# Kernel tuning notes

Hardware: AMD Instinct MI355X
Metric: run time of the kernel (lower is better)

## Reference

```python
import jax, jax.numpy as jnp
import numpy as np

B, T, M, C, H = 2, 2048, 512, 512, 8
D = C // H
SCALE = 1.0 / np.sqrt(D).astype(np.float32)


def _linear_params(key, din, dout):
    kw, kb = jax.random.split(key)
    W = jax.random.normal(kw, (din, dout), jnp.float32) * 0.02
    b = jax.random.normal(kb, (dout,), jnp.float32) * 0.02
    return W, b


def setup_inputs() -> dict:
    key = jax.random.key(0)
    ks = jax.random.split(key, 8)
    x = jax.random.normal(ks[0], (B, T, C), jnp.float32)
    y = jax.random.normal(ks[1], (B, M, C), jnp.float32)
    # causal mask over the x (self / product-attn) axis, broadcasts to [B,H,T,T]
    attn_x_mask = jnp.tril(jnp.ones((T, T), jnp.int32))[None, None]
    Wqkv_x, bqkv_x = _linear_params(ks[2], C, 3 * C)
    Wqkv_y, bqkv_y = _linear_params(ks[3], C, 3 * C)
    Wgs, bgs = _linear_params(ks[4], C, C)
    Wgc, bgc = _linear_params(ks[5], C, C)
    Wp, bp = _linear_params(ks[6], C, C)
    return dict(x=x, y=y, attn_x_mask=attn_x_mask,
                Wqkv_x=Wqkv_x, bqkv_x=bqkv_x, Wqkv_y=Wqkv_y, bqkv_y=bqkv_y,
                Wgs=Wgs, bgs=bgs, Wgc=Wgc, bgc=bgc, Wp=Wp, bp=bp)


def _heads(t, L):
    # [B,L,C] -> [B,H,L,D]
    return t.reshape(B, L, H, D).transpose(0, 2, 1, 3)


def reference(x, y, attn_x_mask, Wqkv_x, bqkv_x, Wqkv_y, bqkv_y,
              Wgs, bgs, Wgc, bgc, Wp, bp):
    neg_inf = jnp.float32(-jnp.inf)
    qx, kx, vx = jnp.split(x @ Wqkv_x + bqkv_x, 3, axis=-1)
    qy, ky, vy = jnp.split(y @ Wqkv_y + bqkv_y, 3, axis=-1)
    q_x, k_x, v_x = _heads(qx, T), _heads(kx, T), _heads(vx, T)
    q_y, k_y, v_y = _heads(qy, M), _heads(ky, M), _heads(vy, M)

    # cross attention x -> y : [B,H,T,M]
    catt_x2y = jnp.einsum('bhtd,bhmd->bhtm', q_x, k_y) * SCALE
    cval_x2y = jnp.einsum('bhtm,bhmd->bhtd', jax.nn.softmax(catt_x2y, axis=-1), v_y)
    cval_x2y = cval_x2y.transpose(0, 2, 1, 3).reshape(B, T, C)

    # product attention: (x->y scores) @ (y->x scores) : [B,H,T,T]
    catt_y2x = jnp.einsum('bhmd,bhtd->bhmt', q_y, k_x) * SCALE
    prod = jnp.einsum('bhtm,bhms->bhts', catt_x2y, catt_y2x) * SCALE
    prod = jnp.where(attn_x_mask == 0, neg_inf, prod)
    cval_y2x = jnp.einsum('bhts,bhsd->bhtd', jax.nn.softmax(prod, axis=-1), v_x)
    cval_y2x = cval_y2x.transpose(0, 2, 1, 3).reshape(B, T, C)

    cval = cval_x2y + cval_y2x

    # self attention on x : [B,H,T,T]
    satt = jnp.einsum('bhtd,bhsd->bhts', q_x, k_x) * SCALE
    satt = jnp.where(attn_x_mask == 0, neg_inf, satt)
    sval = jnp.einsum('bhts,bhsd->bhtd', jax.nn.softmax(satt, axis=-1), v_x)
    sval = sval.transpose(0, 2, 1, 3).reshape(B, T, C)

    sgate = jax.nn.sigmoid(sval @ Wgs + bgs)
    cgate = jax.nn.sigmoid(cval @ Wgc + bgc)
    out = (sgate * cval + cgate * sval) @ Wp + bp
    return out
```

## Files before the change

### kernel.cpp

```cpp
#include <hip/hip_runtime.h>
#include <hip/hip_bf16.h>

typedef unsigned short ushort_t;
typedef __attribute__((ext_vector_type(8))) short s8v;
typedef __attribute__((ext_vector_type(4))) float f4;
typedef __attribute__((ext_vector_type(4))) unsigned short u16x4;

#define BB 2
#define TT 2048
#define MMM 512
#define CC 512
#define HH 8
#define DD 64
#define SCALE 0.125f
#define SCALE_L2E 0.18033688011112042f

__device__ __forceinline__ ushort_t f2bf(float v) {
    __hip_bfloat16 h = __float2bfloat16(v);
    return *reinterpret_cast<ushort_t*>(&h);
}
__device__ __forceinline__ float bf2f(ushort_t u) {
    __hip_bfloat16 h;
    *reinterpret_cast<ushort_t*>(&h) = u;
    return __bfloat162float(h);
}
__device__ __forceinline__ float exp2_raw(float v) {
    float p;
    asm("v_exp_f32 %0, %1" : "=v"(p) : "v"(v));
    return p;
}

__device__ __forceinline__ void gload16(const void* g, void* l) {
    __builtin_amdgcn_global_load_lds((const __attribute__((address_space(1))) void*)g,
                                     (__attribute__((address_space(3))) void*)l, 16, 0, 0);
}

__device__ __forceinline__ void transp32(const float* W, ushort_t* WT, int K, int N,
                                         int bx, int by, int tid) {
    const int k0 = by * 32, n0 = bx * 32;
    __shared__ float t[32][33];
    for (int i = tid; i < 1024; i += 256) {
        int r = i >> 5, c = i & 31;
        t[r][c] = W[(long)(k0 + r) * N + n0 + c];
    }
    __syncthreads();
    for (int i = tid; i < 1024; i += 256) {
        int r = i >> 5, c = i & 31;
        WT[(long)(n0 + r) * K + k0 + c] = f2bf(t[c][r]);
    }
}
__device__ __forceinline__ void cvt4(const float* s, ushort_t* d, long blk, int tid) {
    long i = (blk * 256 + tid) * 4;
    float4 v = *(const float4*)(s + i);
    u16x4 o;
    o[0] = f2bf(v.x); o[1] = f2bf(v.y); o[2] = f2bf(v.z); o[3] = f2bf(v.w);
    *(u16x4*)(d + i) = o;
}

__global__ __launch_bounds__(256) void prep_k(
    const float* __restrict__ x, const float* __restrict__ y,
    const float* __restrict__ Wqx, const float* __restrict__ Wqy,
    const float* __restrict__ Wgs, const float* __restrict__ Wgc,
    const float* __restrict__ Wp,
    ushort_t* __restrict__ xb, ushort_t* __restrict__ yb,
    ushort_t* __restrict__ WqxT, ushort_t* __restrict__ WqyT,
    ushort_t* __restrict__ WgsT, ushort_t* __restrict__ WgcT,
    ushort_t* __restrict__ WpT)
{
    const int bid = blockIdx.x, tid = threadIdx.x;
    if (bid < 2048)      cvt4(x, xb, bid, tid);
    else if (bid < 2560) cvt4(y, yb, bid - 2048, tid);
    else if (bid < 3328) { int l = bid - 2560; transp32(Wqx, WqxT, 512, 1536, l % 48, l / 48, tid); }
    else if (bid < 4096) { int l = bid - 3328; transp32(Wqy, WqyT, 512, 1536, l % 48, l / 48, tid); }
    else if (bid < 4352) { int l = bid - 4096; transp32(Wgs, WgsT, 512, 512, l % 16, l / 16, tid); }
    else if (bid < 4608) { int l = bid - 4352; transp32(Wgc, WgcT, 512, 512, l % 16, l / 16, tid); }
    else                 { int l = bid - 4608; transp32(Wp, WpT, 512, 512, l % 16, l / 16, tid); }
}

__global__ __launch_bounds__(256) void vT_fused(
    const ushort_t* __restrict__ qkvx, const ushort_t* __restrict__ qkvy,
    ushort_t* __restrict__ vxT, ushort_t* __restrict__ vyT,
    ushort_t* __restrict__ kyT, ushort_t* __restrict__ qyT)
{
    const int bx = blockIdx.x, z = blockIdx.y, b = z >> 3, h = z & 7;
    const ushort_t* src; ushort_t* dst; int S, s0; long sB, dZ;
    if (bx < 32)      { src = qkvx + 1024; dst = vxT; S = TT;  sB = (long)TT * 1536;  dZ = (long)64 * TT;  s0 = bx * 64; }
    else if (bx < 40) { src = qkvy + 1024; dst = vyT; S = MMM; sB = (long)MMM * 1536; dZ = (long)64 * MMM; s0 = (bx - 32) * 64; }
    else if (bx < 48) { src = qkvy + 512;  dst = kyT; S = MMM; sB = (long)MMM * 1536; dZ = (long)64 * MMM; s0 = (bx - 40) * 64; }
    else              { src = qkvy;        dst = qyT; S = MMM; sB = (long)MMM * 1536; dZ = (long)64 * MMM; s0 = (bx - 48) * 64; }
    const ushort_t* sp = src + (long)b * sB + (long)h * 64;
    ushort_t* dp = dst + (long)z * dZ;
    __shared__ ushort_t t[64][65];
    for (int i = threadIdx.x; i < 4096; i += 256) {
        int r = i >> 6, c = i & 63;
        t[r][c] = sp[(long)(s0 + r) * 1536 + c];
    }
    __syncthreads();
    for (int i = threadIdx.x; i < 4096; i += 256) {
        int d = i >> 6, c = i & 63;
        dp[(long)d * S + s0 + c] = t[c][d];
    }
}

__global__ __launch_bounds__(256) void qkv_k(
    const ushort_t* __restrict__ xb, const ushort_t* __restrict__ yb,
    const ushort_t* __restrict__ WqxT, const ushort_t* __restrict__ WqyT,
    const float* __restrict__ bqx, const float* __restrict__ bqy,
    ushort_t* __restrict__ qkvx, ushort_t* __restrict__ qkvy)
{
    const int by = blockIdx.y;
    const ushort_t* A; const ushort_t* Bm; const float* bias; ushort_t* O;
    int r0, qcols;
    if (by < 32) { A = xb; Bm = WqxT; bias = bqx; O = qkvx; r0 = by * 128; qcols = 512; }
    else         { A = yb; Bm = WqyT; bias = bqy; O = qkvy; r0 = (by - 32) * 128; qcols = 0; }
    const int c0 = blockIdx.x * 128;
    const int tid = threadIdx.x, w = tid >> 6, lane = tid & 63;
    const int quad = lane >> 4, l15 = lane & 15;
    const int rowBase = (w >> 1) * 64, colBase = (w & 1) * 64;

    __shared__ __align__(16) ushort_t Al[128 * 64];
    __shared__ __align__(16) ushort_t Bl[128 * 64];

    f4 acc[4][4] = {};

    for (int k0 = 0; k0 < 512; k0 += 64) {
        __syncthreads();
        for (int n = 0; n < 4; ++n) {
            int f = w * 4096 + n * 1024 + lane * 16;
            int row = f >> 7;
            int blk_g = ((f & 127) >> 4) ^ (row & 7);
            gload16(A + (long)(r0 + row) * 512 + k0 + blk_g * 8,
                    &Al[(w * 4096 + n * 1024) >> 1]);
            gload16(Bm + (long)(c0 + row) * 512 + k0 + blk_g * 8,
                    &Bl[(w * 4096 + n * 1024) >> 1]);
        }
        __syncthreads();
#pragma unroll
        for (int ks = 0; ks < 2; ++ks) {
            s8v af[4], bfr[4];
#pragma unroll
            for (int i = 0; i < 4; ++i) {
                int row = rowBase + 16 * i + l15;
                af[i] = *(const s8v*)&Al[row * 64 + (((ks * 4 + quad) ^ (row & 7)) * 8)];
                int col = colBase + 16 * i + l15;
                bfr[i] = *(const s8v*)&Bl[col * 64 + (((ks * 4 + quad) ^ (col & 7)) * 8)];
            }
#pragma unroll
            for (int i = 0; i < 4; ++i)
#pragma unroll
                for (int j = 0; j < 4; ++j)
                    acc[i][j] = __builtin_amdgcn_mfma_f32_16x16x32_bf16(af[i], bfr[j], acc[i][j], 0, 0, 0);
        }
    }

#pragma unroll
    for (int i = 0; i < 4; ++i)
#pragma unroll
        for (int j = 0; j < 4; ++j)
#pragma unroll
            for (int r = 0; r < 4; ++r) {
                int row = r0 + rowBase + 16 * i + quad * 4 + r;
                int col = c0 + colBase + 16 * j + l15;
                float v = acc[i][j][r] + bias[col];
                if (col < qcols) v *= SCALE_L2E;
                O[(long)row * 1536 + col] = f2bf(v);
            }
}

__global__ __launch_bounds__(256) void proj_k(
    const ushort_t* __restrict__ A, const ushort_t* __restrict__ Bm,
    float* __restrict__ O, const float* __restrict__ bias)
{
    const int r0 = blockIdx.y * 128, c0 = blockIdx.x * 64;
    const int tid = threadIdx.x, w = tid >> 6, lane = tid & 63;
    const int quad = lane >> 4, l15 = lane & 15;
    const int rowBase = (w >> 1) * 64, colBase = (w & 1) * 32;

    __shared__ __align__(16) ushort_t Al[128 * 64];
    __shared__ __align__(16) ushort_t Bl[64 * 64];

    f4 acc[4][2] = {};

    for (int k0 = 0; k0 < 512; k0 += 64) {
        __syncthreads();
#pragma unroll
        for (int n = 0; n < 4; ++n) {
            int f = w * 4096 + n * 1024 + lane * 16;
            int row = f >> 7;
            int blk_g = ((f & 127) >> 4) ^ (row & 7);
            gload16(A + (long)(r0 + row) * 512 + k0 + blk_g * 8,
                    &Al[(w * 4096 + n * 1024) >> 1]);
        }
#pragma unroll
        for (int n = 0; n < 2; ++n) {
            int f = w * 2048 + n * 1024 + lane * 16;
            int row = f >> 7;
            int blk_g = ((f & 127) >> 4) ^ (row & 7);
            gload16(Bm + (long)(c0 + row) * 512 + k0 + blk_g * 8,
                    &Bl[(w * 2048 + n * 1024) >> 1]);
        }
        __syncthreads();
#pragma unroll
        for (int ks = 0; ks < 2; ++ks) {
            s8v af[4], bfr[2];
#pragma unroll
            for (int i = 0; i < 4; ++i) {
                int row = rowBase + 16 * i + l15;
                af[i] = *(const s8v*)&Al[row * 64 + (((ks * 4 + quad) ^ (row & 7)) * 8)];
            }
#pragma unroll
            for (int j = 0; j < 2; ++j) {
                int col = colBase + 16 * j + l15;
                bfr[j] = *(const s8v*)&Bl[col * 64 + (((ks * 4 + quad) ^ (col & 7)) * 8)];
            }
#pragma unroll
            for (int i = 0; i < 4; ++i)
#pragma unroll
                for (int j = 0; j < 2; ++j)
                    acc[i][j] = __builtin_amdgcn_mfma_f32_16x16x32_bf16(af[i], bfr[j], acc[i][j], 0, 0, 0);
        }
    }

#pragma unroll
    for (int i = 0; i < 4; ++i)
#pragma unroll
        for (int j = 0; j < 2; ++j)
#pragma unroll
            for (int r = 0; r < 4; ++r) {
                int row = r0 + rowBase + 16 * i + quad * 4 + r;
                int col = c0 + colBase + 16 * j + l15;
                O[(long)row * 512 + col] = acc[i][j][r] + bias[col];
            }
}

__global__ __launch_bounds__(256) void gt_k(const ushort_t* __restrict__ qyT,
                                            const ushort_t* __restrict__ kyT,
                                            ushort_t* __restrict__ Gt)
{
    const int z = blockIdx.x;
    const int tid = threadIdx.x, w = tid >> 6, lane = tid & 63;
    const int quad = lane >> 4, l15 = lane & 15;
    const ushort_t* A  = qyT + (long)z * 64 * MMM;
    const ushort_t* Bm = kyT + (long)z * 64 * MMM;
    __shared__ float red[4][4096];
    f4 acc[4][4] = {};
    for (int kk = 0; kk < 4; ++kk) {
        const int ks = w * 4 + kk;
        s8v af[4], bfr[4];
#pragma unroll
        for (int i = 0; i < 4; ++i) {
            af[i]  = *(const s8v*)(A  + (long)(16 * i + l15) * MMM + ks * 32 + quad * 8);
            bfr[i] = *(const s8v*)(Bm + (long)(16 * i + l15) * MMM + ks * 32 + quad * 8);
        }
#pragma unroll
        for (int i = 0; i < 4; ++i)
#pragma unroll
            for (int j = 0; j < 4; ++j)
                acc[i][j] = __builtin_amdgcn_mfma_f32_16x16x32_bf16(af[i], bfr[j], acc[i][j], 0, 0, 0);
    }
#pragma unroll
    for (int i = 0; i < 4; ++i)
#pragma unroll
        for (int j = 0; j < 4; ++j)
            *(f4*)&red[w][(i * 4 + j) * 256 + lane * 4] = acc[i][j];
    __syncthreads();
    const float s2 = SCALE * SCALE;
#pragma unroll
    for (int j = 0; j < 4; ++j) {
        f4 s = *(const f4*)&red[0][(w * 4 + j) * 256 + lane * 4];
#pragma unroll
        for (int ww = 1; ww < 4; ++ww)
            s += *(const f4*)&red[ww][(w * 4 + j) * 256 + lane * 4];
#pragma unroll
        for (int r = 0; r < 4; ++r) {
            int d2 = 16 * w + quad * 4 + r, d1 = 16 * j + l15;
            Gt[(long)z * 4096 + d2 * 64 + d1] = f2bf(s2 * s[r]);
        }
    }
}

__device__ __forceinline__ void stage_k64(const ushort_t* src, long rstride, int s0,
                                          ushort_t* Kl, int w, int lane) {
#pragma unroll
    for (int n = 0; n < 2; ++n) {
        int f = w * 2048 + n * 1024 + lane * 16;
        int row = f >> 7;
        int krow = ((row & 15) << 2) | (row >> 4);
        int blk = ((f & 127) >> 4) ^ (row & 7);
        gload16(src + (long)(s0 + krow) * rstride + blk * 8, &Kl[(w * 2048 + n * 1024) >> 1]);
    }
}
__device__ __forceinline__ void stage_v64(const ushort_t* src, long rstride, int s0,
                                          ushort_t* Vl, int w, int lane) {
#pragma unroll
    for (int n = 0; n < 2; ++n) {
        int f = w * 2048 + n * 1024 + lane * 16;
        int row = f >> 7;
        int blk = ((f & 127) >> 4) ^ (row & 7);
        gload16(src + (long)row * rstride + s0 + blk * 8, &Vl[(w * 2048 + n * 1024) >> 1]);
    }
}
__device__ __forceinline__ void qk8(f4 Sc[4], const s8v qf[2], const ushort_t* Kl,
                                    int quad, int l15) {
    __builtin_amdgcn_s_setprio(1);
#pragma unroll
    for (int ks = 0; ks < 2; ++ks)
#pragma unroll
        for (int c = 0; c < 4; ++c) {
            int row = 16 * c + l15;
            s8v bb = *(const s8v*)&Kl[row * 64 + (((ks * 4 + quad) ^ (row & 7)) * 8)];
            Sc[c] = __builtin_amdgcn_mfma_f32_16x16x32_bf16(qf[ks], bb, Sc[c], 0, 0, 0);
        }
    __builtin_amdgcn_s_setprio(0);
}
__device__ __forceinline__ void qk8_dual(f4 Ss[4], f4 Sp[4], const s8v qa[2], const s8v qb[2],
                                         const ushort_t* Kl, int quad, int l15) {
    __builtin_amdgcn_s_setprio(1);
#pragma unroll
    for (int ks = 0; ks < 2; ++ks)
#pragma unroll
        for (int c = 0; c < 4; ++c) {
            int row = 16 * c + l15;
            s8v bb = *(const s8v*)&Kl[row * 64 + (((ks * 4 + quad) ^ (row & 7)) * 8)];
            Ss[c] = __builtin_amdgcn_mfma_f32_16x16x32_bf16(qa[ks], bb, Ss[c], 0, 0, 0);
            Sp[c] = __builtin_amdgcn_mfma_f32_16x16x32_bf16(qb[ks], bb, Sp[c], 0, 0, 0);
        }
    __builtin_amdgcn_s_setprio(0);
}
__device__ __forceinline__ void smax0(const f4 Sc[4], float l_i[4], ushort_t* PlW,
                                      int diag, int trow0, int s0, int quad, int l15) {
#pragma unroll
    for (int r = 0; r < 4; ++r) {
        const int trow = trow0 + quad * 4 + r;
        u16x4 o;
#pragma unroll
        for (int c = 0; c < 4; ++c) {
            float v = Sc[c][r];
            if (diag && (s0 + 4 * l15 + c) > trow) v = -3e38f;
            float p = exp2_raw(v);
            l_i[r] += p;
            o[c] = f2bf(p);
        }
        *(u16x4*)&PlW[(quad * 4 + r) * 72 + 4 * l15] = o;
    }
}
__device__ __forceinline__ void pv8(f4 Oc[4], const ushort_t* PlW, const ushort_t* Vl,
                                    int quad, int l15) {
    __builtin_amdgcn_s_setprio(1);
#pragma unroll
    for (int ks = 0; ks < 2; ++ks) {
        s8v a = *(const s8v*)&PlW[l15 * 72 + ks * 32 + quad * 8];
#pragma unroll
        for (int c = 0; c < 4; ++c) {
            int row = 16 * c + l15;
            s8v bb = *(const s8v*)&Vl[row * 64 + (((ks * 4 + quad) ^ (row & 7)) * 8)];
            Oc[c] = __builtin_amdgcn_mfma_f32_16x16x32_bf16(a, bb, Oc[c], 0, 0, 0);
        }
    }
    __builtin_amdgcn_s_setprio(0);
}
__device__ __forceinline__ void pv8_dual(f4 Os[4], f4 Op[4], const ushort_t* Ps,
                                         const ushort_t* Pp, const ushort_t* Vl,
                                         int quad, int l15) {
    __builtin_amdgcn_s_setprio(1);
#pragma unroll
    for (int ks = 0; ks < 2; ++ks) {
        s8v as = *(const s8v*)&Ps[l15 * 72 + ks * 32 + quad * 8];
        s8v ap = *(const s8v*)&Pp[l15 * 72 + ks * 32 + quad * 8];
#pragma unroll
        for (int c = 0; c < 4; ++c) {
            int row = 16 * c + l15;
            s8v bb = *(const s8v*)&Vl[row * 64 + (((ks * 4 + quad) ^ (row & 7)) * 8)];
            Os[c] = __builtin_amdgcn_mfma_f32_16x16x32_bf16(as, bb, Os[c], 0, 0, 0);
            Op[c] = __builtin_amdgcn_mfma_f32_16x16x32_bf16(ap, bb, Op[c], 0, 0, 0);
        }
    }
    __builtin_amdgcn_s_setprio(0);
}

__global__ __launch_bounds__(256, 2) void flash_fused(
    const ushort_t* __restrict__ qkvx, const ushort_t* __restrict__ qkvy,
    const ushort_t* __restrict__ Gt, const ushort_t* __restrict__ vxT,
    const ushort_t* __restrict__ vyT,
    ushort_t* __restrict__ cval, ushort_t* __restrict__ sval)
{
    const int z = blockIdx.y, b = z >> 3, h = z & 7;
    const ushort_t* qx = qkvx + (long)b * (TT * 1536) + h * 64;
    const ushort_t* kx = qx + 512;
    const ushort_t* ky = qkvy + (long)b * (MMM * 1536) + 512 + h * 64;
    const ushort_t* Gz = Gt + (long)z * 4096;
    const ushort_t* vx = vxT + (long)z * (64 * TT);
    const ushort_t* vy = vyT + (long)z * (64 * MMM);

    const int xw = (z & 8) ? (int)blockIdx.x : (int)(gridDim.x - 1 - blockIdx.x);
    const int t0 = xw * 64;
    const int tid = threadIdx.x, w = tid >> 6, lane = tid & 63;
    const int quad = lane >> 4, l15 = lane & 15;

    __shared__ __align__(16) ushort_t Kl[2][64 * 64];
    __shared__ __align__(16) ushort_t Vl[2][64 * 64];
    __shared__ __align__(16) ushort_t Pl[2][4 * 16 * 72];
    ushort_t* PlWs = &Pl[0][w * 1152];
    ushort_t* PlWp = &Pl[1][w * 1152];

    stage_k64(ky, 1536, 0, Kl[0], w, lane);
    stage_v64(vy, MMM, 0, Vl[0], w, lane);

    const int qrow = t0 + 16 * w + l15;
    s8v qfx[2], qft[2];
    qfx[0] = *(const s8v*)(qx + (long)qrow * 1536 + quad * 8);
    qfx[1] = *(const s8v*)(qx + (long)qrow * 1536 + 32 + quad * 8);
    {
        f4 qa[4] = {};
#pragma unroll
        for (int ks = 0; ks < 2; ++ks)
#pragma unroll
            for (int j = 0; j < 4; ++j) {
                s8v bb = *(const s8v*)(Gz + (4 * l15 + j) * 64 + ks * 32 + quad * 8);
                qa[j] = __builtin_amdgcn_mfma_f32_16x16x32_bf16(qfx[ks], bb, qa[j], 0, 0, 0);
            }
#pragma unroll
        for (int r = 0; r < 4; ++r) {
            u16x4 o;
#pragma unroll
            for (int j = 0; j < 4; ++j) o[j] = f2bf(qa[j][r]);
            *(u16x4*)&PlWs[(quad * 4 + r) * 72 + 4 * l15] = o;
        }
        qft[0] = *(const s8v*)&PlWs[l15 * 72 + quad * 8];
        qft[1] = *(const s8v*)&PlWs[l15 * 72 + 32 + quad * 8];
    }

    f4 Occ[4] = {}, Ocs[4] = {}, Ocp[4] = {};
    float lc[4] = {}, ls[4] = {}, lp[4] = {};

    const int nT1 = MMM / 64;
    const int nTiles = nT1 + t0 / 64 + 1;

    for (int ti = 0; ti < nTiles; ++ti) {
        const int bi = ti & 1;
        __syncthreads();
        if (ti + 1 < nTiles) {
            const int tn = ti + 1, bn = tn & 1;
            if (tn < nT1) {
                stage_k64(ky, 1536, tn * 64, Kl[bn], w, lane);
                stage_v64(vy, MMM, tn * 64, Vl[bn], w, lane);
            } else {
                const int s0n = (tn - nT1) * 64;
                stage_k64(kx, 1536, s0n, Kl[bn], w, lane);
                stage_v64(vx, TT, s0n, Vl[bn], w, lane);
            }
        }
        if (ti < nT1) {
            f4 Sc[4] = {};
            qk8(Sc, qfx, Kl[bi], quad, l15);
            smax0(Sc, lc, PlWs, 0, 0, 0, quad, l15);
            pv8(Occ, PlWs, Vl[bi], quad, l15);
        } else {
            const int s0 = (ti - nT1) * 64;
            const int diag = (s0 == t0);
            f4 Ss[4] = {}, Sp[4] = {};
            qk8_dual(Ss, Sp, qfx, qft, Kl[bi], quad, l15);
            smax0(Ss, ls, PlWs, diag, t0 + 16 * w, s0, quad, l15);
            smax0(Sp, lp, PlWp, diag, t0 + 16 * w, s0, quad, l15);
            pv8_dual(Ocs, Ocp, PlWs, PlWp, Vl[bi], quad, l15);
        }
    }

#pragma unroll
    for (int r = 0; r < 4; ++r)
#pragma unroll
        for (int mb = 1; mb < 16; mb <<= 1) {
            lc[r] += __shfl_xor(lc[r], mb, 64);
            ls[r] += __shfl_xor(ls[r], mb, 64);
            lp[r] += __shfl_xor(lp[r], mb, 64);
        }

    const long ob = (long)b * (TT * CC) + h * 64;
#pragma unroll
    for (int r = 0; r < 4; ++r) {
        int row = t0 + 16 * w + quad * 4 + r;
        float ic = 1.f / lc[r], ip = 1.f / lp[r], isv = 1.f / ls[r];
#pragma unroll
        for (int c = 0; c < 4; ++c) {
            long idx = ob + (long)row * CC + 16 * c + l15;
            cval[idx] = f2bf(Occ[c][r] * ic + Ocp[c][r] * ip);
            sval[idx] = f2bf(Ocs[c][r] * isv);
        }
    }
}

__global__ __launch_bounds__(256) void gate_gemm(
    const ushort_t* __restrict__ sval, const ushort_t* __restrict__ cvalb,
    const ushort_t* __restrict__ WgsT, const ushort_t* __restrict__ WgcT,
    const float* __restrict__ bgs, const float* __restrict__ bgc,
    ushort_t* __restrict__ tmpb)
{
    const int r0 = blockIdx.y * 128, c0 = blockIdx.x * 64;
    const int tid = threadIdx.x, w = tid >> 6, lane = tid & 63;
    const int quad = lane >> 4, l15 = lane & 15;
    const int rowBase = (w >> 1) * 64, colBase = (w & 1) * 32;

    __shared__ __align__(16) ushort_t Al[128 * 64];
    __shared__ __align__(16) ushort_t Bl[64 * 64];

    f4 acc1[4][2] = {}, acc2[4][2] = {};

    for (int pass = 0; pass < 2; ++pass) {
        const ushort_t* A = pass ? cvalb : sval;
        const ushort_t* Bm = pass ? WgcT : WgsT;
        for (int k0 = 0; k0 < 512; k0 += 64) {
            __syncthreads();
#pragma unroll
            for (int n = 0; n < 4; ++n) {
                int f = w * 4096 + n * 1024 + lane * 16;
                int row = f >> 7;
                int blk_g = ((f & 127) >> 4) ^ (row & 7);
                gload16(A + (long)(r0 + row) * 512 + k0 + blk_g * 8,
                        &Al[(w * 4096 + n * 1024) >> 1]);
            }
#pragma unroll
            for (int n = 0; n < 2; ++n) {
                int f = w * 2048 + n * 1024 + lane * 16;
                int row = f >> 7;
                int blk_g = ((f & 127) >> 4) ^ (row & 7);
                gload16(Bm + (long)(c0 + row) * 512 + k0 + blk_g * 8,
                        &Bl[(w * 2048 + n * 1024) >> 1]);
            }
            __syncthreads();
#pragma unroll
            for (int ks = 0; ks < 2; ++ks) {
                s8v af[4], bfr[2];
#pragma unroll
                for (int i = 0; i < 4; ++i) {
                    int row = rowBase + 16 * i + l15;
                    af[i] = *(const s8v*)&Al[row * 64 + (((ks * 4 + quad) ^ (row & 7)) * 8)];
                }
#pragma unroll
                for (int j = 0; j < 2; ++j) {
                    int col = colBase + 16 * j + l15;
                    bfr[j] = *(const s8v*)&Bl[col * 64 + (((ks * 4 + quad) ^ (col & 7)) * 8)];
                }
                if (pass == 0) {
#pragma unroll
                    for (int i = 0; i < 4; ++i)
#pragma unroll
                        for (int j = 0; j < 2; ++j)
                            acc1[i][j] = __builtin_amdgcn_mfma_f32_16x16x32_bf16(af[i], bfr[j], acc1[i][j], 0, 0, 0);
                } else {
#pragma unroll
                    for (int i = 0; i < 4; ++i)
#pragma unroll
                        for (int j = 0; j < 2; ++j)
                            acc2[i][j] = __builtin_amdgcn_mfma_f32_16x16x32_bf16(af[i], bfr[j], acc2[i][j], 0, 0, 0);
                }
            }
        }
    }

#pragma unroll
    for (int i = 0; i < 4; ++i)
#pragma unroll
        for (int j = 0; j < 2; ++j)
#pragma unroll
            for (int r = 0; r < 4; ++r) {
                int row = r0 + rowBase + 16 * i + quad * 4 + r;
                int col = c0 + colBase + 16 * j + l15;
                long idx = (long)row * 512 + col;
                float g1 = 1.f / (1.f + __expf(-(acc1[i][j][r] + bgs[col])));
                float g2 = 1.f / (1.f + __expf(-(acc2[i][j][r] + bgc[col])));
                tmpb[idx] = f2bf(g1 * bf2f(cvalb[idx]) + g2 * bf2f(sval[idx]));
            }
}

extern "C" void kernel_launch(void* const* d_in, const int* in_sizes, int n_in,
                              void* d_out, int out_size, void* d_ws, size_t ws_size,
                              hipStream_t stream) {
    const float* x      = (const float*)d_in[0];
    const float* y      = (const float*)d_in[1];
    const float* Wqkv_x = (const float*)d_in[3];
    const float* bqkv_x = (const float*)d_in[4];
    const float* Wqkv_y = (const float*)d_in[5];
    const float* bqkv_y = (const float*)d_in[6];
    const float* Wgs    = (const float*)d_in[7];
    const float* bgs    = (const float*)d_in[8];
    const float* Wgc    = (const float*)d_in[9];
    const float* bgc    = (const float*)d_in[10];
    const float* Wp     = (const float*)d_in[11];
    const float* bp     = (const float*)d_in[12];
    float* out = (float*)d_out;

    ushort_t* u = (ushort_t*)d_ws;
    long o = 0;
    ushort_t* xb    = u + o; o += (long)BB * TT * CC;
    ushort_t* yb    = u + o; o += (long)BB * MMM * CC;
    ushort_t* WqxT  = u + o; o += 1536L * 512;
    ushort_t* WqyT  = u + o; o += 1536L * 512;
    ushort_t* WgsT  = u + o; o += 512L * 512;
    ushort_t* WgcT  = u + o; o += 512L * 512;
    ushort_t* WpT   = u + o; o += 512L * 512;
    ushort_t* qkvx  = u + o; o += (long)BB * TT * 1536;
    ushort_t* qkvy  = u + o; o += (long)BB * MMM * 1536;
    ushort_t* vxT   = u + o; o += (long)BB * HH * DD * TT;
    ushort_t* vyT   = u + o; o += (long)BB * HH * DD * MMM;
    ushort_t* kyT   = u + o; o += (long)BB * HH * DD * MMM;
    ushort_t* qyT   = u + o; o += (long)BB * HH * DD * MMM;
    ushort_t* Gt    = u + o; o += 16L * 64 * 64;
    ushort_t* cvalb = u + o; o += (long)BB * TT * CC;
    ushort_t* sval  = u + o; o += (long)BB * TT * CC;
    ushort_t* tmpb  = u + o; o += (long)BB * TT * CC;

    dim3 blk(256);

    prep_k<<<dim3(4864), blk, 0, stream>>>(x, y, Wqkv_x, Wqkv_y, Wgs, Wgc, Wp,
                                           xb, yb, WqxT, WqyT, WgsT, WgcT, WpT);

    qkv_k<<<dim3(12, 40), blk, 0, stream>>>(xb, yb, WqxT, WqyT, bqkv_x, bqkv_y, qkvx, qkvy);

    vT_fused<<<dim3(56, 16), blk, 0, stream>>>(qkvx, qkvy, vxT, vyT, kyT, qyT);

    gt_k<<<dim3(16), blk, 0, stream>>>(qyT, kyT, Gt);

    flash_fused<<<dim3(32, 16), blk, 0, stream>>>(qkvx, qkvy, Gt, vxT, vyT, cvalb, sval);

    gate_gemm<<<dim3(8, 32), blk, 0, stream>>>(sval, cvalb, WgsT, WgcT, bgs, bgc, tmpb);

    proj_k<<<dim3(8, 32), blk, 0, stream>>>(tmpb, WpT, out, bp);
}
```

Measured before the change: 214.5 us.

## Pipeline GEMM and flash-attention staging with multi-buffered LDS and vectorized transposes

Adds double buffering to the QKV GEMM and triple-buffered LDS prefetch to the flash, gate and projection kernels. These use explicit vmcnt waits and raw barriers so global loads overlap MFMA work. The gate and projection GEMMs shrink to 64x64 tiles, doubling the grid to fill more CUs. The V/K/Q transpose kernel now uses 16-byte vector loads and stores with an XOR-swizzled LDS tile. More LDS per block may lower occupancy, and the hand-written vmcnt counts depend on the exact number of loads issued per stage.

```diff
diff --git a/kernel.cpp b/kernel.cpp
--- a/kernel.cpp
+++ b/kernel.cpp
@@ -90,15 +90,48 @@
     else              { src = qkvy;        dst = qyT; S = MMM; sB = (long)MMM * 1536; dZ = (long)64 * MMM; s0 = (bx - 48) * 64; }
     const ushort_t* sp = src + (long)b * sB + (long)h * 64;
     ushort_t* dp = dst + (long)z * dZ;
-    __shared__ ushort_t t[64][65];
-    for (int i = threadIdx.x; i < 4096; i += 256) {
-        int r = i >> 6, c = i & 63;
-        t[r][c] = sp[(long)(s0 + r) * 1536 + c];
+    __shared__ __align__(16) ushort_t t[64][80];
+    const int tid = threadIdx.x;
+#pragma unroll
+    for (int p = 0; p < 2; ++p) {
+        int id = tid + p * 256;
+        int r = id >> 3, cc = (id & 7) * 8;
+        int cs = cc ^ ((r >> 3) * 8);
+        *(s8v*)&t[r][cs] = *(const s8v*)&sp[(long)(s0 + r) * 1536 + cc];
     }
     __syncthreads();
-    for (int i = threadIdx.x; i < 4096; i += 256) {
-        int d = i >> 6, c = i & 63;
-        dp[(long)d * S + s0 + c] = t[c][d];
+#pragma unroll
+    for (int p = 0; p < 2; ++p) {
+        int id = tid + p * 256;
+        int d = id >> 3, cc = (id & 7) * 8;
+        s8v o;
+#pragma unroll
+        for (int k = 0; k < 8; ++k) {
+            int r = cc + k;
+            o[k] = (short)t[r][d ^ ((r >> 3) * 8)];
+        }
+        *(s8v*)&dp[(long)d * S + s0 + cc] = o;
+    }
+}
+
+__device__ __forceinline__ void stage_rows128(const ushort_t* src, long k0,
+                                              ushort_t* dstL, int w, int lane) {
+#pragma unroll
+    for (int n = 0; n < 4; ++n) {
+        int f = w * 4096 + n * 1024 + lane * 16;
+        int row = f >> 7;
+        int blk_g = ((f & 127) >> 4) ^ (row & 7);
+        gload16(src + (long)row * 512 + k0 + blk_g * 8, dstL + ((w * 4096 + n * 1024) >> 1));
+    }
+}
+__device__ __forceinline__ void stage_rows64(const ushort_t* src, long k0,
+                                             ushort_t* dstL, int w, int lane) {
+#pragma unroll
+    for (int n = 0; n < 2; ++n) {
+        int f = w * 2048 + n * 1024 + lane * 16;
+        int row = f >> 7;
+        int blk_g = ((f & 127) >> 4) ^ (row & 7);
+        gload16(src + (long)row * 512 + k0 + blk_g * 8, dstL + ((w * 2048 + n * 1024) >> 1));
     }
 }
 
@@ -118,32 +151,33 @@
     const int quad = lane >> 4, l15 = lane & 15;
     const int rowBase = (w >> 1) * 64, colBase = (w & 1) * 64;
 
-    __shared__ __align__(16) ushort_t Al[128 * 64];
-    __shared__ __align__(16) ushort_t Bl[128 * 64];
+    __shared__ __align__(16) ushort_t Al[2][128 * 64];
+    __shared__ __align__(16) ushort_t Bl[2][128 * 64];
+
+    const ushort_t* Ab = A + (long)r0 * 512;
+    const ushort_t* Bb = Bm + (long)c0 * 512;
 
     f4 acc[4][4] = {};
 
-    for (int k0 = 0; k0 < 512; k0 += 64) {
-        __syncthreads();
-        for (int n = 0; n < 4; ++n) {
-            int f = w * 4096 + n * 1024 + lane * 16;
-            int row = f >> 7;
-            int blk_g = ((f & 127) >> 4) ^ (row & 7);
-            gload16(A + (long)(r0 + row) * 512 + k0 + blk_g * 8,
-                    &Al[(w * 4096 + n * 1024) >> 1]);
-            gload16(Bm + (long)(c0 + row) * 512 + k0 + blk_g * 8,
-                    &Bl[(w * 4096 + n * 1024) >> 1]);
-        }
-        __syncthreads();
+    stage_rows128(Ab, 0, Al[0], w, lane);
+    stage_rows128(Bb, 0, Bl[0], w, lane);
+    __syncthreads();
+
+    for (int kk = 0; kk < 8; ++kk) {
+        const int cur = kk & 1;
+        if (kk < 7) {
+            stage_rows128(Ab, (kk + 1) * 64, Al[cur ^ 1], w, lane);
+            stage_rows128(Bb, (kk + 1) * 64, Bl[cur ^ 1], w, lane);
+        }
 #pragma unroll
         for (int ks = 0; ks < 2; ++ks) {
             s8v af[4], bfr[4];
 #pragma unroll
             for (int i = 0; i < 4; ++i) {
                 int row = rowBase + 16 * i + l15;
-                af[i] = *(const s8v*)&Al[row * 64 + (((ks * 4 + quad) ^ (row & 7)) * 8)];
+                af[i] = *(const s8v*)&Al[cur][row * 64 + (((ks * 4 + quad) ^ (row & 7)) * 8)];
                 int col = colBase + 16 * i + l15;
-                bfr[i] = *(const s8v*)&Bl[col * 64 + (((ks * 4 + quad) ^ (col & 7)) * 8)];
+                bfr[i] = *(const s8v*)&Bl[cur][col * 64 + (((ks * 4 + quad) ^ (col & 7)) * 8)];
             }
 #pragma unroll
             for (int i = 0; i < 4; ++i)
@@ -151,6 +185,7 @@
                 for (int j = 0; j < 4; ++j)
                     acc[i][j] = __builtin_amdgcn_mfma_f32_16x16x32_bf16(af[i], bfr[j], acc[i][j], 0, 0, 0);
         }
+        __syncthreads();
     }
 
 #pragma unroll
@@ -171,58 +206,55 @@
     const ushort_t* __restrict__ A, const ushort_t* __restrict__ Bm,
     float* __restrict__ O, const float* __restrict__ bias)
 {
-    const int r0 = blockIdx.y * 128, c0 = blockIdx.x * 64;
+    const int r0 = blockIdx.y * 64, c0 = blockIdx.x * 64;
     const int tid = threadIdx.x, w = tid >> 6, lane = tid & 63;
     const int quad = lane >> 4, l15 = lane & 15;
-    const int rowBase = (w >> 1) * 64, colBase = (w & 1) * 32;
-
-    __shared__ __align__(16) ushort_t Al[128 * 64];
-    __shared__ __align__(16) ushort_t Bl[64 * 64];
-
-    f4 acc[4][2] = {};
-
-    for (int k0 = 0; k0 < 512; k0 += 64) {
-        __syncthreads();
-#pragma unroll
-        for (int n = 0; n < 4; ++n) {
-            int f = w * 4096 + n * 1024 + lane * 16;
-            int row = f >> 7;
-            int blk_g = ((f & 127) >> 4) ^ (row & 7);
-            gload16(A + (long)(r0 + row) * 512 + k0 + blk_g * 8,
-                    &Al[(w * 4096 + n * 1024) >> 1]);
-        }
-#pragma unroll
-        for (int n = 0; n < 2; ++n) {
-            int f = w * 2048 + n * 1024 + lane * 16;
-            int row = f >> 7;
-            int blk_g = ((f & 127) >> 4) ^ (row & 7);
-            gload16(Bm + (long)(c0 + row) * 512 + k0 + blk_g * 8,
-                    &Bl[(w * 2048 + n * 1024) >> 1]);
-        }
-        __syncthreads();
+    const int rowBase = (w >> 1) * 32, colBase = (w & 1) * 32;
+
+    __shared__ __align__(16) ushort_t Al[3][64 * 64];
+    __shared__ __align__(16) ushort_t Bl[3][64 * 64];
+
+    const ushort_t* Ab = A + (long)r0 * 512;
+    const ushort_t* Bb = Bm + (long)c0 * 512;
+
+    f4 acc[2][2] = {};
+
+    stage_rows64(Ab, 0, Al[0], w, lane);
+    stage_rows64(Bb, 0, Bl[0], w, lane);
+    stage_rows64(Ab, 64, Al[1], w, lane);
+    stage_rows64(Bb, 64, Bl[1], w, lane);
+
+    int cur = 0;
+    for (int kk = 0; kk < 8; ++kk) {
+        if (kk + 1 < 8) asm volatile("s_waitcnt vmcnt(4)" ::: "memory");
+        else            asm volatile("s_waitcnt vmcnt(0)" ::: "memory");
+        asm volatile("s_barrier" ::: "memory");
+        if (kk + 2 < 8) {
+            int s = cur + 2; if (s >= 3) s -= 3;
+            stage_rows64(Ab, (kk + 2) * 64, Al[s], w, lane);
+            stage_rows64(Bb, (kk + 2) * 64, Bl[s], w, lane);
+        }
 #pragma unroll
         for (int ks = 0; ks < 2; ++ks) {
-            s8v af[4], bfr[2];
-#pragma unroll
-            for (int i = 0; i < 4; ++i) {
+            s8v af[2], bfr[2];
+#pragma unroll
+            for (int i = 0; i < 2; ++i) {
                 int row = rowBase + 16 * i + l15;
-                af[i] = *(const s8v*)&Al[row * 64 + (((ks * 4 + quad) ^ (row & 7)) * 8)];
-            }
-#pragma unroll
-            for (int j = 0; j < 2; ++j) {
-                int col = colBase + 16 * j + l15;
-                bfr[j] = *(const s8v*)&Bl[col * 64 + (((ks * 4 + quad) ^ (col & 7)) * 8)];
-            }
-#pragma unroll
-            for (int i = 0; i < 4; ++i)
+                af[i] = *(const s8v*)&Al[cur][row * 64 + (((ks * 4 + quad) ^ (row & 7)) * 8)];
+                int col = colBase + 16 * i + l15;
+                bfr[i] = *(const s8v*)&Bl[cur][col * 64 + (((ks * 4 + quad) ^ (col & 7)) * 8)];
+            }
+#pragma unroll
+            for (int i = 0; i < 2; ++i)
 #pragma unroll
                 for (int j = 0; j < 2; ++j)
                     acc[i][j] = __builtin_amdgcn_mfma_f32_16x16x32_bf16(af[i], bfr[j], acc[i][j], 0, 0, 0);
         }
-    }
-
-#pragma unroll
-    for (int i = 0; i < 4; ++i)
+        if (++cur == 3) cur = 0;
+    }
+
+#pragma unroll
+    for (int i = 0; i < 2; ++i)
 #pragma unroll
         for (int j = 0; j < 2; ++j)
 #pragma unroll
@@ -397,14 +429,16 @@
     const int tid = threadIdx.x, w = tid >> 6, lane = tid & 63;
     const int quad = lane >> 4, l15 = lane & 15;
 
-    __shared__ __align__(16) ushort_t Kl[2][64 * 64];
-    __shared__ __align__(16) ushort_t Vl[2][64 * 64];
+    __shared__ __align__(16) ushort_t Kl[3][64 * 64];
+    __shared__ __align__(16) ushort_t Vl[3][64 * 64];
     __shared__ __align__(16) ushort_t Pl[2][4 * 16 * 72];
     ushort_t* PlWs = &Pl[0][w * 1152];
     ushort_t* PlWp = &Pl[1][w * 1152];
 
     stage_k64(ky, 1536, 0, Kl[0], w, lane);
     stage_v64(vy, MMM, 0, Vl[0], w, lane);
+    stage_k64(ky, 1536, 64, Kl[1], w, lane);
+    stage_v64(vy, MMM, 64, Vl[1], w, lane);
 
     const int qrow = t0 + 16 * w + l15;
     s8v qfx[2], qft[2];
@@ -436,34 +470,38 @@
     const int nT1 = MMM / 64;
     const int nTiles = nT1 + t0 / 64 + 1;
 
+    int cur = 0;
     for (int ti = 0; ti < nTiles; ++ti) {
-        const int bi = ti & 1;
-        __syncthreads();
-        if (ti + 1 < nTiles) {
-            const int tn = ti + 1, bn = tn & 1;
+        if (ti + 1 < nTiles) asm volatile("s_waitcnt vmcnt(4)" ::: "memory");
+        else                 asm volatile("s_waitcnt vmcnt(0)" ::: "memory");
+        asm volatile("s_barrier" ::: "memory");
+        if (ti + 2 < nTiles) {
+            int s = cur + 2; if (s >= 3) s -= 3;
+            const int tn = ti + 2;
             if (tn < nT1) {
-                stage_k64(ky, 1536, tn * 64, Kl[bn], w, lane);
-                stage_v64(vy, MMM, tn * 64, Vl[bn], w, lane);
+                stage_k64(ky, 1536, tn * 64, Kl[s], w, lane);
+                stage_v64(vy, MMM, tn * 64, Vl[s], w, lane);
             } else {
                 const int s0n = (tn - nT1) * 64;
-                stage_k64(kx, 1536, s0n, Kl[bn], w, lane);
-                stage_v64(vx, TT, s0n, Vl[bn], w, lane);
+                stage_k64(kx, 1536, s0n, Kl[s], w, lane);
+                stage_v64(vx, TT, s0n, Vl[s], w, lane);
             }
         }
         if (ti < nT1) {
             f4 Sc[4] = {};
-            qk8(Sc, qfx, Kl[bi], quad, l15);
+            qk8(Sc, qfx, Kl[cur], quad, l15);
             smax0(Sc, lc, PlWs, 0, 0, 0, quad, l15);
-            pv8(Occ, PlWs, Vl[bi], quad, l15);
+            pv8(Occ, PlWs, Vl[cur], quad, l15);
         } else {
             const int s0 = (ti - nT1) * 64;
             const int diag = (s0 == t0);
             f4 Ss[4] = {}, Sp[4] = {};
-            qk8_dual(Ss, Sp, qfx, qft, Kl[bi], quad, l15);
+            qk8_dual(Ss, Sp, qfx, qft, Kl[cur], quad, l15);
             smax0(Ss, ls, PlWs, diag, t0 + 16 * w, s0, quad, l15);
             smax0(Sp, lp, PlWp, diag, t0 + 16 * w, s0, quad, l15);
-            pv8_dual(Ocs, Ocp, PlWs, PlWp, Vl[bi], quad, l15);
-        }
+            pv8_dual(Ocs, Ocp, PlWs, PlWp, Vl[cur], quad, l15);
+        }
+        if (++cur == 3) cur = 0;
     }
 
 #pragma unroll
@@ -495,70 +533,64 @@
     const float* __restrict__ bgs, const float* __restrict__ bgc,
     ushort_t* __restrict__ tmpb)
 {
-    const int r0 = blockIdx.y * 128, c0 = blockIdx.x * 64;
+    const int r0 = blockIdx.y * 64, c0 = blockIdx.x * 64;
     const int tid = threadIdx.x, w = tid >> 6, lane = tid & 63;
     const int quad = lane >> 4, l15 = lane & 15;
-    const int rowBase = (w >> 1) * 64, colBase = (w & 1) * 32;
-
-    __shared__ __align__(16) ushort_t Al[128 * 64];
-    __shared__ __align__(16) ushort_t Bl[64 * 64];
-
-    f4 acc1[4][2] = {}, acc2[4][2] = {};
-
-    for (int pass = 0; pass < 2; ++pass) {
-        const ushort_t* A = pass ? cvalb : sval;
-        const ushort_t* Bm = pass ? WgcT : WgsT;
-        for (int k0 = 0; k0 < 512; k0 += 64) {
-            __syncthreads();
-#pragma unroll
-            for (int n = 0; n < 4; ++n) {
-                int f = w * 4096 + n * 1024 + lane * 16;
-                int row = f >> 7;
-                int blk_g = ((f & 127) >> 4) ^ (row & 7);
-                gload16(A + (long)(r0 + row) * 512 + k0 + blk_g * 8,
-                        &Al[(w * 4096 + n * 1024) >> 1]);
-            }
-#pragma unroll
-            for (int n = 0; n < 2; ++n) {
-                int f = w * 2048 + n * 1024 + lane * 16;
-                int row = f >> 7;
-                int blk_g = ((f & 127) >> 4) ^ (row & 7);
-                gload16(Bm + (long)(c0 + row) * 512 + k0 + blk_g * 8,
-                        &Bl[(w * 2048 + n * 1024) >> 1]);
-            }
-            __syncthreads();
-#pragma unroll
-            for (int ks = 0; ks < 2; ++ks) {
-                s8v af[4], bfr[2];
-#pragma unroll
-                for (int i = 0; i < 4; ++i) {
-                    int row = rowBase + 16 * i + l15;
-                    af[i] = *(const s8v*)&Al[row * 64 + (((ks * 4 + quad) ^ (row & 7)) * 8)];
-                }
-#pragma unroll
-                for (int j = 0; j < 2; ++j) {
-                    int col = colBase + 16 * j + l15;
-                    bfr[j] = *(const s8v*)&Bl[col * 64 + (((ks * 4 + quad) ^ (col & 7)) * 8)];
-                }
-                if (pass == 0) {
-#pragma unroll
-                    for (int i = 0; i < 4; ++i)
-#pragma unroll
-                        for (int j = 0; j < 2; ++j)
-                            acc1[i][j] = __builtin_amdgcn_mfma_f32_16x16x32_bf16(af[i], bfr[j], acc1[i][j], 0, 0, 0);
-                } else {
-#pragma unroll
-                    for (int i = 0; i < 4; ++i)
-#pragma unroll
-                        for (int j = 0; j < 2; ++j)
-                            acc2[i][j] = __builtin_amdgcn_mfma_f32_16x16x32_bf16(af[i], bfr[j], acc2[i][j], 0, 0, 0);
-                }
-            }
-        }
-    }
-
-#pragma unroll
-    for (int i = 0; i < 4; ++i)
+    const int rowBase = (w >> 1) * 32, colBase = (w & 1) * 32;
+
+    __shared__ __align__(16) ushort_t Al[3][64 * 64];
+    __shared__ __align__(16) ushort_t Bl[3][64 * 64];
+
+    const ushort_t* Ap[2] = { sval + (long)r0 * 512, cvalb + (long)r0 * 512 };
+    const ushort_t* Bp[2] = { WgsT + (long)c0 * 512, WgcT + (long)c0 * 512 };
+
+    f4 acc1[2][2] = {}, acc2[2][2] = {};
+
+    stage_rows64(Ap[0], 0, Al[0], w, lane);
+    stage_rows64(Bp[0], 0, Bl[0], w, lane);
+    stage_rows64(Ap[0], 64, Al[1], w, lane);
+    stage_rows64(Bp[0], 64, Bl[1], w, lane);
+
+    int cur = 0;
+    for (int st = 0; st < 16; ++st) {
+        if (st + 1 < 16) asm volatile("s_waitcnt vmcnt(4)" ::: "memory");
+        else             asm volatile("s_waitcnt vmcnt(0)" ::: "memory");
+        asm volatile("s_barrier" ::: "memory");
+        if (st + 2 < 16) {
+            int s = cur + 2; if (s >= 3) s -= 3;
+            const int nx = st + 2, p = nx >> 3;
+            stage_rows64(Ap[p], (nx & 7) * 64, Al[s], w, lane);
+            stage_rows64(Bp[p], (nx & 7) * 64, Bl[s], w, lane);
+        }
+#pragma unroll
+        for (int ks = 0; ks < 2; ++ks) {
+            s8v af[2], bfr[2];
+#pragma unroll
+            for (int i = 0; i < 2; ++i) {
+                int row = rowBase + 16 * i + l15;
+                af[i] = *(const s8v*)&Al[cur][row * 64 + (((ks * 4 + quad) ^ (row & 7)) * 8)];
+                int col = colBase + 16 * i + l15;
+                bfr[i] = *(const s8v*)&Bl[cur][col * 64 + (((ks * 4 + quad) ^ (col & 7)) * 8)];
+            }
+            if (st < 8) {
+#pragma unroll
+                for (int i = 0; i < 2; ++i)
+#pragma unroll
+                    for (int j = 0; j < 2; ++j)
+                        acc1[i][j] = __builtin_amdgcn_mfma_f32_16x16x32_bf16(af[i], bfr[j], acc1[i][j], 0, 0, 0);
+            } else {
+#pragma unroll
+                for (int i = 0; i < 2; ++i)
+#pragma unroll
+                    for (int j = 0; j < 2; ++j)
+                        acc2[i][j] = __builtin_amdgcn_mfma_f32_16x16x32_bf16(af[i], bfr[j], acc2[i][j], 0, 0, 0);
+            }
+        }
+        if (++cur == 3) cur = 0;
+    }
+
+#pragma unroll
+    for (int i = 0; i < 2; ++i)
 #pragma unroll
         for (int j = 0; j < 2; ++j)
 #pragma unroll
@@ -622,7 +654,7 @@
 
     flash_fused<<<dim3(32, 16), blk, 0, stream>>>(qkvx, qkvy, Gt, vxT, vyT, cvalb, sval);
 
-    gate_gemm<<<dim3(8, 32), blk, 0, stream>>>(sval, cvalb, WgsT, WgcT, bgs, bgc, tmpb);
-
-    proj_k<<<dim3(8, 32), blk, 0, stream>>>(tmpb, WpT, out, bp);
-}
+    gate_gemm<<<dim3(8, 64), blk, 0, stream>>>(sval, cvalb, WgsT, WgcT, bgs, bgc, tmpb);
+
+    proj_k<<<dim3(8, 64), blk, 0, stream>>>(tmpb, WpT, out, bp);
+}
```

Measured after the change: 206.6 us. 1.04x faster.
